# Performance work log

Hardware: AMD Instinct MI355X
Metric: run time of the kernel (lower is better)

## Reference

```python
import jax, jax.numpy as jnp
import numpy as np

N, E, IN_DIM, HID, OUT = 50000, 800000, 128, 128, 64


def setup_inputs() -> dict:
    key = jax.random.key(0)
    k = jax.random.split(key, 6)
    h = jax.random.normal(k[0], (N, IN_DIM), dtype=jnp.float32)
    edge_index = jax.random.randint(k[1], (2, E), 0, N, dtype=jnp.int64)
    s_in, s_hid = 1.0 / np.sqrt(IN_DIM), 1.0 / np.sqrt(HID)
    W_gcn = jax.random.uniform(k[2], (IN_DIM, HID), jnp.float32, -s_in, s_in)
    b_gcn = jnp.zeros((HID,), jnp.float32)
    W_fc = jax.random.uniform(k[3], (HID, OUT), jnp.float32, -s_hid, s_hid)
    b_fc = jax.random.uniform(k[4], (OUT,), jnp.float32, -s_hid, s_hid)
    return {"h": h, "edge_index": edge_index, "W_gcn": W_gcn,
            "b_gcn": b_gcn, "W_fc": W_fc, "b_fc": b_fc}


def reference(h, edge_index, W_gcn, b_gcn, W_fc, b_fc):
    n = h.shape[0]
    # GCNConv: transform, add self-loops, symmetric normalization, scatter-add
    x = h @ W_gcn                                   # [N, HID]
    loop = jnp.arange(n, dtype=edge_index.dtype)
    row = jnp.concatenate([edge_index[0], loop])    # source nodes
    col = jnp.concatenate([edge_index[1], loop])    # destination nodes
    deg = jax.ops.segment_sum(jnp.ones_like(col, dtype=x.dtype), col,
                              num_segments=n)       # in-degree incl. self-loop
    dinv = jnp.where(deg > 0, jax.lax.rsqrt(deg), 0.0)
    norm = dinv[row] * dinv[col]                    # [E+N]
    msg = x[row] * norm[:, None]                    # gather + scale
    agg = jax.ops.segment_sum(msg, col, num_segments=n) + b_gcn
    # ReLU then projection
    return jax.nn.relu(agg) @ W_fc + b_fc
```

## Files before the change

kernel.cpp:

```cpp
#include <hip/hip_runtime.h>

#define N_NODES 50000
#define N_EDGES 800000
#define NBKT 782
#define BINB 196
#define CASTB 391
#define BCAP 1792
#define UTS 136

typedef __attribute__((ext_vector_type(4))) float floatx4;
typedef __attribute__((ext_vector_type(8))) _Float16 half8;
typedef __attribute__((ext_vector_type(4))) _Float16 half4;
typedef __attribute__((ext_vector_type(2))) _Float16 half2v;

#define O_GF    0UL
#define O_DEG   3200UL
#define O_W1    203264UL
#define O_W2    236032UL
#define O_STG   252416UL
#define O_H16   5857792UL

__global__ __launch_bounds__(256) void k_bin(const int* __restrict__ ei,
                                             const float* __restrict__ h,
                                             int* __restrict__ gfill,
                                             unsigned* __restrict__ staging,
                                             const float* __restrict__ Wg,
                                             const float* __restrict__ Wf,
                                             _Float16* __restrict__ W1,
                                             _Float16* __restrict__ W2,
                                             _Float16* __restrict__ h16) {
    int b = blockIdx.x, t = threadIdx.x;
    if (b >= BINB + 96) {
        int wb = b - (BINB + 96);
        int nb = wb * 128;
        int nn = min(128, N_NODES - nb);
        if (nn <= 0) return;
        const floatx4* src = (const floatx4*)(h + (size_t)nb * 128);
        half4* dst = (half4*)(h16 + (size_t)nb * 128);
        int nq = nn * 32;
        for (int i = t; i < nq; i += 256) {
            floatx4 v = src[i];
            half4 o;
            o[0] = (_Float16)v[0]; o[1] = (_Float16)v[1];
            o[2] = (_Float16)v[2]; o[3] = (_Float16)v[3];
            dst[i] = o;
        }
        return;
    }
    if (b >= BINB) {
        int wb = b - BINB;
        if (wb < 64) {
            int i = wb * 256 + t;
            int n = i >> 7, k = i & 127;
            W1[i] = (_Float16)Wg[k * 128 + n];
        } else {
            int i = (wb - 64) * 256 + t;
            int n = i >> 7, k = i & 127;
            W2[i] = (_Float16)Wf[k * 64 + n];
        }
        return;
    }
    __shared__ int cnt[NBKT];
    __shared__ int gbase[NBKT];
    __shared__ int s_i64;
    if (t < 64) {
        unsigned w = ((const unsigned*)ei)[2 * t + 1];
        unsigned long long m = __ballot(w == 0u);
        if (t == 0) s_i64 = (__popcll(m) >= 60) ? 1 : 0;
    }
    for (int i = t; i < NBKT; i += 256) cnt[i] = 0;
    __syncthreads();
    bool i64 = s_i64 != 0;
    int e0 = b * 4096 + t * 16;
    int sv[16], dvv[16];
    if (i64) {
        const int4* ps = (const int4*)(ei) + (e0 >> 1);
        const int4* pd = (const int4*)(ei + 2 * (size_t)N_EDGES) + (e0 >> 1);
#pragma unroll
        for (int g = 0; g < 8; ++g) {
            if (e0 + 2 * g < N_EDGES) {
                int4 s4 = ps[g], d4 = pd[g];
                sv[2 * g] = s4.x; sv[2 * g + 1] = s4.z;
                dvv[2 * g] = d4.x; dvv[2 * g + 1] = d4.z;
            } else { dvv[2 * g] = -1; dvv[2 * g + 1] = -1; }
        }
    } else {
        const int4* ps = (const int4*)(ei) + (e0 >> 2);
        const int4* pd = (const int4*)(ei + (size_t)N_EDGES) + (e0 >> 2);
#pragma unroll
        for (int g = 0; g < 4; ++g) {
            if (e0 + 4 * g < N_EDGES) {
                int4 s4 = ps[g], d4 = pd[g];
                sv[4 * g] = s4.x; sv[4 * g + 1] = s4.y; sv[4 * g + 2] = s4.z; sv[4 * g + 3] = s4.w;
                dvv[4 * g] = d4.x; dvv[4 * g + 1] = d4.y; dvv[4 * g + 2] = d4.z; dvv[4 * g + 3] = d4.w;
            } else { dvv[4 * g] = -1; dvv[4 * g + 1] = -1; dvv[4 * g + 2] = -1; dvv[4 * g + 3] = -1; }
        }
    }
    unsigned pk[16]; int rk[16]; short bk[16];
#pragma unroll
    for (int j = 0; j < 16; ++j) {
        int d = dvv[j];
        if (d >= 0 && e0 + j < N_EDGES) {
            int bkt = d >> 6;
            bk[j] = (short)bkt;
            pk[j] = (unsigned)sv[j] | ((unsigned)(d & 63) << 16);
            rk[j] = atomicAdd(&cnt[bkt], 1);
        } else bk[j] = -1;
    }
    __syncthreads();
    for (int i = t; i < NBKT; i += 256)
        gbase[i] = atomicAdd(&gfill[i], cnt[i]);
    __syncthreads();
#pragma unroll
    for (int j = 0; j < 16; ++j) {
        if (bk[j] >= 0) {
            int pos = gbase[bk[j]] + rk[j];
            if (pos < BCAP) staging[(size_t)bk[j] * BCAP + pos] = pk[j];
        }
    }
}

__global__ __launch_bounds__(256) void k_deg(const int* __restrict__ gfill,
                                             const unsigned* __restrict__ staging,
                                             int* __restrict__ deg_g) {
    __shared__ int deg[128];
    int b = blockIdx.x, t = threadIdx.x;
    int nb = b * 128;
    int nn = min(128, N_NODES - nb);
    if (nn <= 0) return;
    if (t < 128) deg[t] = 0;
    __syncthreads();
#pragma unroll
    for (int kb = 0; kb < 2; ++kb) {
        int gb = b * 2 + kb;
        int cnt = min(gfill[gb], BCAP);
        const unsigned* st = staging + (size_t)gb * BCAP;
        for (int i = t; i < cnt; i += 256)
            atomicAdd(&deg[kb * 64 + (st[i] >> 16)], 1);
    }
    __syncthreads();
    if (t < nn) deg_g[nb + t] = deg[t];
}

__global__ __launch_bounds__(256, 8) void k_aggF(const _Float16* __restrict__ h16,
                                                 const int* __restrict__ gfill,
                                                 const unsigned* __restrict__ staging,
                                                 const int* __restrict__ deg_g,
                                                 const _Float16* __restrict__ W1,
                                                 const _Float16* __restrict__ W2,
                                                 const float* __restrict__ bg,
                                                 const float* __restrict__ bfc,
                                                 float* __restrict__ out) {
    __shared__ _Float16 ut[16 * UTS];
    __shared__ _Float16 z[16 * UTS];
    __shared__ unsigned se32[BCAP];
    __shared__ int deg16[16], seg16[16], cur16[16];
    __shared__ float sdv16[16];
    int t = threadIdx.x;
    int wave = t >> 6;
    int lane = t & 63;
    int nb = blockIdx.x * 16;
    int bkt = blockIdx.x >> 2;
    unsigned lo = (unsigned)(blockIdx.x & 3) * 16;
    int cnt = min(gfill[bkt], BCAP);
    if (t < 16) deg16[t] = 0;
    __syncthreads();
    const unsigned* st = staging + (size_t)bkt * BCAP;
    unsigned held[7]; int dgv[7];
#pragma unroll
    for (int r = 0; r < 7; ++r) {
        int i = t + r * 256;
        unsigned p = 0xFFFFFFFFu;
        if (i < cnt) p = st[i];
        unsigned tg = p >> 16;
        dgv[r] = 0;
        if (tg - lo < 16u) {
            atomicAdd(&deg16[tg - lo], 1);
            dgv[r] = deg_g[p & 0xFFFFu];
        } else p = 0xFFFFFFFFu;
        held[r] = p;
    }
    __syncthreads();
    if (t == 0) {
        int s = 0;
#pragma unroll
        for (int k = 0; k < 16; ++k) { seg16[k] = s; cur16[k] = s; s += deg16[k]; }
    }
    if (t < 16) sdv16[t] = rsqrtf((float)(deg16[t] + 1));
    __syncthreads();
#pragma unroll
    for (int r = 0; r < 7; ++r) {
        unsigned p = held[r];
        if (p != 0xFFFFFFFFu) {
            int rk = atomicAdd(&cur16[(p >> 16) - lo], 1);
            if (rk < BCAP) se32[rk] = ((unsigned)dgv[r] << 16) | (p & 0xFFFFu);
        }
    }
    __syncthreads();
    for (int q = 0; q < 4; ++q) {
        int tag = wave * 4 + q;
        int node = nb + tag;
        int p0 = seg16[tag];
        int p1 = p0 + deg16[tag];
        float sc = sdv16[tag];
        half2v us = *(const half2v*)(h16 + (size_t)node * 128 + lane * 2);
        float a0 = (float)us[0] * sc, a1 = (float)us[1] * sc;
        for (int base = p0; base < p1; base += 64) {
            int c = p1 - base; if (c > 64) c = 64;
            int idx = 0;
            if (lane < c) idx = (int)se32[base + lane];
            float wf = rsqrtf((float)((unsigned)idx >> 16) + 1.f);
            int j = 0;
            for (; j + 8 <= c; j += 8) {
                int s0 = __shfl(idx, j),     s1 = __shfl(idx, j + 1);
                int s2 = __shfl(idx, j + 2), s3 = __shfl(idx, j + 3);
                int s4 = __shfl(idx, j + 4), s5 = __shfl(idx, j + 5);
                int s6 = __shfl(idx, j + 6), s7 = __shfl(idx, j + 7);
                float f0 = __shfl(wf, j),     f1 = __shfl(wf, j + 1);
                float f2 = __shfl(wf, j + 2), f3 = __shfl(wf, j + 3);
                float f4 = __shfl(wf, j + 4), f5 = __shfl(wf, j + 5);
                float f6 = __shfl(wf, j + 6), f7 = __shfl(wf, j + 7);
                half2v u0 = *(const half2v*)(h16 + (size_t)(s0 & 0xFFFF) * 128 + lane * 2);
                half2v u1 = *(const half2v*)(h16 + (size_t)(s1 & 0xFFFF) * 128 + lane * 2);
                half2v u2 = *(const half2v*)(h16 + (size_t)(s2 & 0xFFFF) * 128 + lane * 2);
                half2v u3 = *(const half2v*)(h16 + (size_t)(s3 & 0xFFFF) * 128 + lane * 2);
                half2v u4 = *(const half2v*)(h16 + (size_t)(s4 & 0xFFFF) * 128 + lane * 2);
                half2v u5 = *(const half2v*)(h16 + (size_t)(s5 & 0xFFFF) * 128 + lane * 2);
                half2v u6 = *(const half2v*)(h16 + (size_t)(s6 & 0xFFFF) * 128 + lane * 2);
                half2v u7 = *(const half2v*)(h16 + (size_t)(s7 & 0xFFFF) * 128 + lane * 2);
                a0 = fmaf((float)u0[0], f0, a0); a1 = fmaf((float)u0[1], f0, a1);
                a0 = fmaf((float)u1[0], f1, a0); a1 = fmaf((float)u1[1], f1, a1);
                a0 = fmaf((float)u2[0], f2, a0); a1 = fmaf((float)u2[1], f2, a1);
                a0 = fmaf((float)u3[0], f3, a0); a1 = fmaf((float)u3[1], f3, a1);
                a0 = fmaf((float)u4[0], f4, a0); a1 = fmaf((float)u4[1], f4, a1);
                a0 = fmaf((float)u5[0], f5, a0); a1 = fmaf((float)u5[1], f5, a1);
                a0 = fmaf((float)u6[0], f6, a0); a1 = fmaf((float)u6[1], f6, a1);
                a0 = fmaf((float)u7[0], f7, a0); a1 = fmaf((float)u7[1], f7, a1);
            }
            for (; j + 4 <= c; j += 4) {
                int s0 = __shfl(idx, j),     s1 = __shfl(idx, j + 1);
                int s2 = __shfl(idx, j + 2), s3 = __shfl(idx, j + 3);
                float f0 = __shfl(wf, j),     f1 = __shfl(wf, j + 1);
                float f2 = __shfl(wf, j + 2), f3 = __shfl(wf, j + 3);
                half2v u0 = *(const half2v*)(h16 + (size_t)(s0 & 0xFFFF) * 128 + lane * 2);
                half2v u1 = *(const half2v*)(h16 + (size_t)(s1 & 0xFFFF) * 128 + lane * 2);
                half2v u2 = *(const half2v*)(h16 + (size_t)(s2 & 0xFFFF) * 128 + lane * 2);
                half2v u3 = *(const half2v*)(h16 + (size_t)(s3 & 0xFFFF) * 128 + lane * 2);
                a0 = fmaf((float)u0[0], f0, a0); a1 = fmaf((float)u0[1], f0, a1);
                a0 = fmaf((float)u1[0], f1, a0); a1 = fmaf((float)u1[1], f1, a1);
                a0 = fmaf((float)u2[0], f2, a0); a1 = fmaf((float)u2[1], f2, a1);
                a0 = fmaf((float)u3[0], f3, a0); a1 = fmaf((float)u3[1], f3, a1);
            }
            for (; j < c; ++j) {
                int s = __shfl(idx, j);
                float f = __shfl(wf, j);
                half2v uu = *(const half2v*)(h16 + (size_t)(s & 0xFFFF) * 128 + lane * 2);
                a0 = fmaf((float)uu[0], f, a0); a1 = fmaf((float)uu[1], f, a1);
            }
        }
        int r = wave * 4 + q;
        ut[r * UTS + lane * 2]     = (_Float16)(a0 * sc);
        ut[r * UTS + lane * 2 + 1] = (_Float16)(a1 * sc);
    }
    __syncthreads();
    int quad = lane >> 4, l15 = lane & 15;
    half8 a[4];
#pragma unroll
    for (int kk = 0; kk < 4; ++kk)
        a[kk] = *(const half8*)(ut + l15 * UTS + kk * 32 + quad * 8);
#pragma unroll
    for (int tt = 0; tt < 2; ++tt) {
        floatx4 acc = {0.f, 0.f, 0.f, 0.f};
        int n = (wave * 2 + tt) * 16 + l15;
#pragma unroll
        for (int kk = 0; kk < 4; ++kk) {
            half8 bb = *(const half8*)(W1 + n * 128 + kk * 32 + quad * 8);
            acc = __builtin_amdgcn_mfma_f32_16x16x32_f16(a[kk], bb, acc, 0, 0, 0);
        }
        float bias = bg[n];
#pragma unroll
        for (int i = 0; i < 4; ++i)
            z[(quad * 4 + i) * UTS + n] = (_Float16)fmaxf(acc[i] + bias, 0.f);
    }
    __syncthreads();
    half8 a2[4];
#pragma unroll
    for (int kk = 0; kk < 4; ++kk)
        a2[kk] = *(const half8*)(z + l15 * UTS + kk * 32 + quad * 8);
    {
        floatx4 acc = {0.f, 0.f, 0.f, 0.f};
        int n = wave * 16 + l15;
#pragma unroll
        for (int kk = 0; kk < 4; ++kk) {
            half8 bb = *(const half8*)(W2 + n * 128 + kk * 32 + quad * 8);
            acc = __builtin_amdgcn_mfma_f32_16x16x32_f16(a2[kk], bb, acc, 0, 0, 0);
        }
        float bias = bfc[n];
#pragma unroll
        for (int i = 0; i < 4; ++i)
            out[(size_t)(nb + quad * 4 + i) * 64 + n] = acc[i] + bias;
    }
}

extern "C" void kernel_launch(void* const* d_in, const int* in_sizes, int n_in,
                              void* d_out, int out_size, void* d_ws, size_t ws_size,
                              hipStream_t stream) {
    (void)in_sizes; (void)n_in; (void)out_size; (void)ws_size;
    const float* h  = (const float*)d_in[0];
    const int*   ei = (const int*)d_in[1];
    const float* Wg = (const float*)d_in[2];
    const float* bg = (const float*)d_in[3];
    const float* Wf = (const float*)d_in[4];
    const float* bf = (const float*)d_in[5];
    float* out = (float*)d_out;

    char* ws = (char*)d_ws;
    int*      gfill = (int*)(ws + O_GF);
    int*      deg_g = (int*)(ws + O_DEG);
    _Float16* W1    = (_Float16*)(ws + O_W1);
    _Float16* W2    = (_Float16*)(ws + O_W2);
    unsigned* staging = (unsigned*)(ws + O_STG);
    _Float16* h16   = (_Float16*)(ws + O_H16);

    hipMemsetAsync(gfill, 0, NBKT * sizeof(int), stream);
    k_bin<<<BINB + 96 + CASTB, 256, 0, stream>>>(ei, h, gfill, staging,
                                                 Wg, Wf, W1, W2, h16);
    k_deg<<<(N_NODES + 127) / 128, 256, 0, stream>>>(gfill, staging, deg_g);
    k_aggF<<<N_NODES / 16, 256, 0, stream>>>(h16, gfill, staging, deg_g,
                                             W1, W2, bg, bf, out);
}
```

Baseline: 151.6 us.

## Fuse degree counting into binning kernel via global atomics, drop k_deg

Removes the separate k_deg kernel and instead has k_bin atomically increment a global per-node in-degree array as it bins each edge. The memset is widened to clear both the bucket fill counters and the degree array. k_aggF now reads its 16 node degrees directly instead of recounting them from the staging buffer, so the staging scan happens only once. This saves a kernel launch and one pass over staging, at the cost of about 800k scattered global atomics in k_bin.

```diff
diff --git a/kernel.cpp b/kernel.cpp
--- a/kernel.cpp
+++ b/kernel.cpp
@@ -23,6 +23,7 @@
 __global__ __launch_bounds__(256) void k_bin(const int* __restrict__ ei,
                                              const float* __restrict__ h,
                                              int* __restrict__ gfill,
+                                             int* __restrict__ deg_g,
                                              unsigned* __restrict__ staging,
                                              const float* __restrict__ Wg,
                                              const float* __restrict__ Wf,
@@ -118,28 +119,11 @@
             if (pos < BCAP) staging[(size_t)bk[j] * BCAP + pos] = pk[j];
         }
     }
-}
-
-__global__ __launch_bounds__(256) void k_deg(const int* __restrict__ gfill,
-                                             const unsigned* __restrict__ staging,
-                                             int* __restrict__ deg_g) {
-    __shared__ int deg[128];
-    int b = blockIdx.x, t = threadIdx.x;
-    int nb = b * 128;
-    int nn = min(128, N_NODES - nb);
-    if (nn <= 0) return;
-    if (t < 128) deg[t] = 0;
-    __syncthreads();
-#pragma unroll
-    for (int kb = 0; kb < 2; ++kb) {
-        int gb = b * 2 + kb;
-        int cnt = min(gfill[gb], BCAP);
-        const unsigned* st = staging + (size_t)gb * BCAP;
-        for (int i = t; i < cnt; i += 256)
-            atomicAdd(&deg[kb * 64 + (st[i] >> 16)], 1);
-    }
-    __syncthreads();
-    if (t < nn) deg_g[nb + t] = deg[t];
+#pragma unroll
+    for (int j = 0; j < 16; ++j) {
+        if (bk[j] >= 0)
+            atomicAdd(&deg_g[((int)bk[j] << 6) | (int)((pk[j] >> 16) & 63u)], 1);
+    }
 }
 
 __global__ __launch_bounds__(256, 8) void k_aggF(const _Float16* __restrict__ h16,
@@ -163,22 +147,10 @@
     int bkt = blockIdx.x >> 2;
     unsigned lo = (unsigned)(blockIdx.x & 3) * 16;
     int cnt = min(gfill[bkt], BCAP);
-    if (t < 16) deg16[t] = 0;
-    __syncthreads();
-    const unsigned* st = staging + (size_t)bkt * BCAP;
-    unsigned held[7]; int dgv[7];
-#pragma unroll
-    for (int r = 0; r < 7; ++r) {
-        int i = t + r * 256;
-        unsigned p = 0xFFFFFFFFu;
-        if (i < cnt) p = st[i];
-        unsigned tg = p >> 16;
-        dgv[r] = 0;
-        if (tg - lo < 16u) {
-            atomicAdd(&deg16[tg - lo], 1);
-            dgv[r] = deg_g[p & 0xFFFFu];
-        } else p = 0xFFFFFFFFu;
-        held[r] = p;
+    if (t < 16) {
+        int dg = deg_g[nb + t];
+        deg16[t] = dg;
+        sdv16[t] = rsqrtf((float)(dg + 1));
     }
     __syncthreads();
     if (t == 0) {
@@ -186,14 +158,16 @@
 #pragma unroll
         for (int k = 0; k < 16; ++k) { seg16[k] = s; cur16[k] = s; s += deg16[k]; }
     }
-    if (t < 16) sdv16[t] = rsqrtf((float)(deg16[t] + 1));
-    __syncthreads();
-#pragma unroll
-    for (int r = 0; r < 7; ++r) {
-        unsigned p = held[r];
-        if (p != 0xFFFFFFFFu) {
-            int rk = atomicAdd(&cur16[(p >> 16) - lo], 1);
-            if (rk < BCAP) se32[rk] = ((unsigned)dgv[r] << 16) | (p & 0xFFFFu);
+    __syncthreads();
+    const unsigned* st = staging + (size_t)bkt * BCAP;
+    for (int i = t; i < cnt; i += 256) {
+        unsigned p = st[i];
+        unsigned tg = (p >> 16) - lo;
+        if (tg < 16u) {
+            int rk = atomicAdd(&cur16[tg], 1);
+            unsigned src = p & 0xFFFFu;
+            unsigned dg = (unsigned)deg_g[src];
+            if (rk < BCAP) se32[rk] = (dg << 16) | src;
         }
     }
     __syncthreads();
@@ -322,10 +296,9 @@
     unsigned* staging = (unsigned*)(ws + O_STG);
     _Float16* h16   = (_Float16*)(ws + O_H16);
 
-    hipMemsetAsync(gfill, 0, NBKT * sizeof(int), stream);
-    k_bin<<<BINB + 96 + CASTB, 256, 0, stream>>>(ei, h, gfill, staging,
+    hipMemsetAsync(ws, 0, O_W1, stream);
+    k_bin<<<BINB + 96 + CASTB, 256, 0, stream>>>(ei, h, gfill, deg_g, staging,
                                                  Wg, Wf, W1, W2, h16);
-    k_deg<<<(N_NODES + 127) / 128, 256, 0, stream>>>(gfill, staging, deg_g);
     k_aggF<<<N_NODES / 16, 256, 0, stream>>>(h16, gfill, staging, deg_g,
                                              W1, W2, bg, bf, out);
 }
```

Result: slower. 178.0 us (+17.4%).
